# Kernel optimization log

Measured on AMD Instinct MI355X. Metric: run time of the kernel, lower is better.

Reference implementation:

```python
import jax, jax.numpy as jnp
import numpy as np

EMBED_DIM = 512
NUM_HEADS = 8
WINDOW = 5
OVERLAP = 1
STRIDE = WINDOW - OVERLAP  # 4


def setup_inputs() -> dict:
    key = jax.random.key(0)
    ks = jax.random.split(key, 5)
    B, S, D = 8, 4096, EMBED_DIM
    s = 1.0 / np.sqrt(D).astype(np.float32)
    return {
        "x": jax.random.normal(ks[0], (B, S, D), jnp.float32),
        "Wq": jax.random.normal(ks[1], (D, D), jnp.float32) * s,
        "bq": jnp.zeros((D,), jnp.float32),
        "Wk": jax.random.normal(ks[2], (D, D), jnp.float32) * s,
        "bk": jnp.zeros((D,), jnp.float32),
        "Wv": jax.random.normal(ks[3], (D, D), jnp.float32) * s,
        "bv": jnp.zeros((D,), jnp.float32),
        "Wo": jax.random.normal(ks[4], (D, D), jnp.float32) * s,
        "bo": jnp.zeros((D,), jnp.float32),
    }


def reference(x, Wq, bq, Wk, bk, Wv, bv, Wo, bo):
    B, S, D = x.shape
    H = NUM_HEADS
    hd = D // H
    pad = (WINDOW - S % WINDOW) % WINDOW
    xp = jnp.pad(x, ((0, 0), (0, pad), (0, 0)))
    P = S + pad
    nw = (P - WINDOW) // STRIDE + 1

    # gather all sliding windows at once: [B, nw, W, D]
    idx = (jnp.arange(nw) * STRIDE)[:, None] + jnp.arange(WINDOW)  # [nw, W]
    win = xp[:, idx]

    def proj(t, W, b):
        return (t @ W + b).reshape(B, nw, WINDOW, H, hd)

    q = proj(win, Wq, bq)
    k = proj(win, Wk, bk)
    v = proj(win, Wv, bv)

    scale = jnp.float32(1.0 / np.sqrt(hd))
    scores = jnp.einsum('bnqhd,bnkhd->bnhqk', q, k) * scale  # [B,nw,H,W,W]
    attn = jax.nn.softmax(scores, axis=-1)
    o = jnp.einsum('bnhqk,bnkhd->bnqhd', attn, v).reshape(B, nw, WINDOW, D)
    o = o @ Wo + bo  # window outputs [B,nw,W,D]

    # overlap-add + count-average (exactly as the torch loop does)
    flat_idx = idx.reshape(-1)
    out = jnp.zeros((B, P, D), jnp.float32).at[:, flat_idx].add(
        o.reshape(B, nw * WINDOW, D))
    counts = jnp.zeros((P,), jnp.float32).at[flat_idx].add(1.0)
    out = out / (counts[None, :, None] + 1e-6)
    out = out[:, :S]

    # torch: sum(all_weights) / num_windows  -> mean over window axis
    attn_weights = attn.mean(axis=1)  # [B, H, W, W]
    return out, attn_weights
```

## Files before the change

### kernel.cpp

```cpp
#include <hip/hip_runtime.h>
#include <hip/hip_bf16.h>


#define SEQ   4096
#define NB    8
#define DIM   512
#define NWIN  1024
#define MTOT  (NB*SEQ)

typedef __bf16 bf16x8 __attribute__((ext_vector_type(8)));
typedef float  f32x4  __attribute__((ext_vector_type(4)));

__device__ __forceinline__ float b2f(unsigned short u) {
  union { unsigned int i; float f; } z; z.i = ((unsigned int)u) << 16; return z.f;
}
__device__ __forceinline__ unsigned short f2b(float f) {
  __bf16 h = (__bf16)f; return __builtin_bit_cast(unsigned short, h);
}
__device__ __forceinline__ void gload_lds16(const void* g, void* l) {
  __builtin_amdgcn_global_load_lds(
      (__attribute__((address_space(1))) void*)g,
      (__attribute__((address_space(3))) void*)l, 16, 0, 0);
}

#define FENCE() asm volatile("" ::: "memory")
#define BAR()   __builtin_amdgcn_s_barrier()
#define VMW8()  asm volatile("s_waitcnt vmcnt(8)" ::: "memory")
#define VMW0()  asm volatile("s_waitcnt vmcnt(0)" ::: "memory")
#define LGK0()  asm volatile("s_waitcnt lgkmcnt(0)" ::: "memory")

__global__ __launch_bounds__(256) void cvt_x(const float* __restrict__ x,
                                             unsigned short* __restrict__ o, int n8) {
  int stride = gridDim.x * blockDim.x;
  for (int i = blockIdx.x * blockDim.x + threadIdx.x; i < n8; i += stride) {
    const float4 a = *(const float4*)(x + (size_t)i * 8);
    const float4 c = *(const float4*)(x + (size_t)i * 8 + 4);
    unsigned short u[8] = {f2b(a.x), f2b(a.y), f2b(a.z), f2b(a.w),
                           f2b(c.x), f2b(c.y), f2b(c.z), f2b(c.w)};
    *(int4*)(o + (size_t)i * 8) = *(const int4*)u;
  }
}

__global__ __launch_bounds__(256) void cvt_w(const float* __restrict__ W0, const float* __restrict__ W1,
                                             const float* __restrict__ W2, const float* __restrict__ W3,
                                             unsigned short* __restrict__ Wt) {
  int i = blockIdx.x * 256 + threadIdx.x;
  int w = i >> 18;
  int r = i & 262143;
  int nn = r >> 9, kk = r & 511;
  const float* W = (w == 0) ? W0 : (w == 1) ? W1 : (w == 2) ? W2 : W3;
  Wt[i] = f2b(W[kk * 512 + nn]);
}

__device__ __forceinline__ void stage_part(int h, const unsigned short* pa, const unsigned short* pb,
    int r0s, int c0s, int r1s, int c1s, char* ldsb, int wid) {
  int kt = h >> 2, slot = (h + 2) & 3;
  int buf = kt & 1, ab = slot >> 1, half = slot & 1;
  const unsigned short* src = ab ? pb : pa;
  int rb = half << 7;
  int kc = kt << 6;
  char* d = ldsb + buf * 65536 + ab * 32768 + half * 16384 + wid * 1024;
  gload_lds16(src + (size_t)(rb + r0s) * 512 + kc + c0s, d);
  gload_lds16(src + (size_t)(rb + r1s) * 512 + kc + c1s, d + 8192);
}

#define LDSB(off) (*(const bf16x8*)(ldsb + (off)))

#define RA4(BUF, HALF) { \
  _Pragma("unroll") for (int mf2 = 0; mf2 < 4; ++mf2) { \
    _Pragma("unroll") for (int ks = 0; ks < 2; ++ks) \
      a[mf2][ks] = LDSB(aS[BUF][ks] + (HALF) * 8192 + mf2 * 2048); } }

#define RB2(BUF, QN) { \
  _Pragma("unroll") for (int nf2 = 0; nf2 < 2; ++nf2) { \
    _Pragma("unroll") for (int ks = 0; ks < 2; ++ks) \
      b[(QN)*2+nf2][ks] = LDSB(bS[BUF][ks] + (QN) * 4096 + nf2 * 2048); } }

#define MMQ(QM, QN) { \
  _Pragma("unroll") for (int ks = 0; ks < 2; ++ks) \
  _Pragma("unroll") for (int mf2 = 0; mf2 < 4; ++mf2) \
  _Pragma("unroll") for (int nf2 = 0; nf2 < 2; ++nf2) \
    acc[(QM)*4+mf2][(QN)*2+nf2] = __builtin_amdgcn_mfma_f32_16x16x32_bf16( \
      a[mf2][ks], b[(QN)*2+nf2][ks], acc[(QM)*4+mf2][(QN)*2+nf2], 0, 0, 0); }

template<int MODE>
__global__ __launch_bounds__(512, 2) void gemm2p(
    const unsigned short* __restrict__ A, const unsigned short* __restrict__ Bw,
    const float* __restrict__ b0, const float* __restrict__ b1, const float* __restrict__ b2,
    unsigned short* __restrict__ o0, unsigned short* __restrict__ o1, unsigned short* __restrict__ o2,
    float* __restrict__ fout) {
  __shared__ unsigned short lds_[65536];
  char* ldsb = (char*)lds_;

  const int nwg = gridDim.x;
  const int cpx = nwg >> 3;
  const int g = blockIdx.x;
  const int sw = (g & 7) * cpx + (g >> 3);
  constexpr int NTN = (MODE == 0) ? 6 : 2;
  const int ntile = sw % NTN, mtile = sw / NTN;
  const int m0 = mtile * 256, n0g = ntile * 256;

  const int tid = threadIdx.x;
  const int lane = tid & 63;
  const int wid = tid >> 6;
  const int wr = wid >> 2, wc = wid & 3;
  const int cl16 = lane & 15, hi = lane >> 4;
  const int hi16 = hi * 16;
  const int sxor = (cl16 & 14) << 3;

  int o0_ = tid * 16;
  int o1_ = 8192 + tid * 16;
  int l0 = o0_ ^ (((o0_ >> 8) & 7) << 4);
  int l1 = o1_ ^ (((o1_ >> 8) & 7) << 4);
  const int r0s = l0 >> 7, c0s = (l0 & 127) >> 1;
  const int r1s = l1 >> 7, c1s = (l1 & 127) >> 1;

  const unsigned short* pa = A + (size_t)m0 * 512;
  const unsigned short* pb = Bw + (size_t)n0g * 512;

  int aS[2][2], bS[2][2];
#pragma unroll
  for (int bu = 0; bu < 2; ++bu)
#pragma unroll
    for (int ks = 0; ks < 2; ++ks) {
      aS[bu][ks] = bu * 65536 + ((wr * 16384 + cl16 * 128 + ks * 64 + hi16) ^ sxor);
      bS[bu][ks] = bu * 65536 + 32768 + (((wc >> 1) * 16384 + (wc & 1) * 8192 + cl16 * 128 + ks * 64 + hi16) ^ sxor);
    }

  f32x4 acc[8][4] = {};
  bf16x8 a[4][2], b[4][2];

#define STG4(KT) { stage_part((KT)*4, pa, pb, r0s, c0s, r1s, c1s, ldsb, wid); \
                   stage_part((KT)*4+1, pa, pb, r0s, c0s, r1s, c1s, ldsb, wid); \
                   stage_part((KT)*4+2, pa, pb, r0s, c0s, r1s, c1s, ldsb, wid); \
                   stage_part((KT)*4+3, pa, pb, r0s, c0s, r1s, c1s, ldsb, wid); }

  STG4(0);

#pragma unroll
  for (int kt = 0; kt < 8; ++kt) {
    const int bu = kt & 1;
    if (kt < 7) { STG4(kt + 1); VMW8(); } else { VMW0(); }
    FENCE(); BAR(); FENCE();
    RB2(bu, 0); RB2(bu, 1);
    RA4(bu, 0);
    MMQ(0, 0); MMQ(0, 1);
    RA4(bu, 1);
    MMQ(1, 1); MMQ(1, 0);
    FENCE(); BAR(); FENCE();
  }

  if constexpr (MODE == 0) {
    const int sel = n0g >> 9;
    const float* bias = (sel == 0) ? b0 : (sel == 1) ? b1 : b2;
    unsigned short* C = (sel == 0) ? o0 : (sel == 1) ? o1 : o2;
    const int lcb = (n0g & 511) + wc * 64;
    unsigned short* wlds = lds_ + wid * 8192;
#pragma unroll
    for (int mf = 0; mf < 8; ++mf)
#pragma unroll
      for (int nf = 0; nf < 4; ++nf) {
        float bv_ = bias[lcb + nf * 16 + cl16];
#pragma unroll
        for (int r = 0; r < 4; ++r) {
          int w = (mf * 16 + hi * 4 + r) * 64 + nf * 16 + cl16;
          wlds[w ^ (((w >> 7) & 7) << 3)] = f2b(acc[mf][nf][r] + bv_);
        }
      }
    LGK0();
#pragma unroll
    for (int itr = 0; itr < 16; ++itr) {
      int f = itr * 512 + lane * 8;
      int row = f >> 6, col = f & 63;
      int4 v = *(const int4*)&wlds[f ^ (((f >> 7) & 7) << 3)];
      *(int4*)(C + (size_t)(m0 + wr * 128 + row) * 512 + lcb + col) = v;
    }
  } else {
#pragma unroll
    for (int nf = 0; nf < 4; ++nf) {
      int ncol = n0g + wc * 64 + nf * 16 + cl16;
      float bv_ = b0[ncol];
#pragma unroll
      for (int mf = 0; mf < 8; ++mf) {
        int rbase = m0 + wr * 128 + mf * 16 + hi * 4;
#pragma unroll
        for (int r = 0; r < 4; ++r) {
          int row = rbase + r;
          int s = row & (SEQ - 1);
          float cnt = ((s & 3) == 0 && s > 0) ? 2.0f : 1.0f;
          fout[(size_t)row * 512 + ncol] = (acc[mf][nf][r] + cnt * bv_) / (cnt + 1e-6f);
        }
      }
    }
  }
}

__global__ __launch_bounds__(256) void attn_win(
    const unsigned short* __restrict__ Qb, const unsigned short* __restrict__ Kb,
    const unsigned short* __restrict__ Vb,
    const float* __restrict__ bq, const float* __restrict__ bk, const float* __restrict__ bv,
    unsigned short* __restrict__ yb, unsigned short* __restrict__ yext,
    float* __restrict__ abuf) {
  const int gw = blockIdx.x * 4 + (threadIdx.x >> 6);
  const int b = gw >> 10, n = gw & (NWIN - 1);
  const int lane = threadIdx.x & 63;
  const int h = lane >> 3, e = lane & 7;
  const int dbase = h * 64 + e * 8;

  float kf[5][8], vf[5][8];
#pragma unroll
  for (int j = 0; j < 5; ++j) {
    int p = 4 * n + j;
    if (p < SEQ) {
      int4 kv = *(const int4*)(Kb + ((size_t)b * SEQ + p) * DIM + dbase);
      int4 vv = *(const int4*)(Vb + ((size_t)b * SEQ + p) * DIM + dbase);
      const unsigned short* kp = (const unsigned short*)&kv;
      const unsigned short* vp = (const unsigned short*)&vv;
#pragma unroll
      for (int d = 0; d < 8; ++d) { kf[j][d] = b2f(kp[d]); vf[j][d] = b2f(vp[d]); }
    } else {
#pragma unroll
      for (int d = 0; d < 8; ++d) { kf[j][d] = bk[dbase + d]; vf[j][d] = bv[dbase + d]; }
    }
  }
  float pm[5][5];
#pragma unroll
  for (int i = 0; i < 5; ++i) {
    int p = 4 * n + i;
    float qf[8];
    if (p < SEQ) {
      int4 qv = *(const int4*)(Qb + ((size_t)b * SEQ + p) * DIM + dbase);
      const unsigned short* qp = (const unsigned short*)&qv;
#pragma unroll
      for (int d = 0; d < 8; ++d) qf[d] = b2f(qp[d]);
    } else {
#pragma unroll
      for (int d = 0; d < 8; ++d) qf[d] = bq[dbase + d];
    }
    float sr[5];
#pragma unroll
    for (int j = 0; j < 5; ++j) {
      float t = 0.f;
#pragma unroll
      for (int d = 0; d < 8; ++d) t += qf[d] * kf[j][d];
      t += __shfl_xor(t, 1);
      t += __shfl_xor(t, 2);
      t += __shfl_xor(t, 4);
      sr[j] = t * 0.125f;
    }
    float mx = sr[0];
#pragma unroll
    for (int j = 1; j < 5; ++j) mx = fmaxf(mx, sr[j]);
    float ex[5], sum = 0.f;
#pragma unroll
    for (int j = 0; j < 5; ++j) { ex[j] = expf(sr[j] - mx); sum += ex[j]; }
    float inv = 1.0f / sum;
#pragma unroll
    for (int j = 0; j < 5; ++j) pm[i][j] = ex[j] * inv;
    float o[8];
#pragma unroll
    for (int d = 0; d < 8; ++d) o[d] = 0.f;
#pragma unroll
    for (int j = 0; j < 5; ++j)
#pragma unroll
      for (int d = 0; d < 8; ++d) o[d] += pm[i][j] * vf[j][d];
    unsigned short u[8];
#pragma unroll
    for (int d = 0; d < 8; ++d) u[d] = f2b(o[d]);
    if (i < 4) {
      *(int4*)(yb + ((size_t)b * SEQ + p) * DIM + dbase) = *(const int4*)u;
    } else {
      *(int4*)(yext + ((size_t)b * NWIN + n) * DIM + dbase) = *(const int4*)u;
    }
  }
  float* ap = abuf + ((size_t)(b * NWIN + n) * 8 + h) * 25;
  if (e == 0) {
#pragma unroll
    for (int i2 = 0; i2 < 5; ++i2)
#pragma unroll
      for (int j2 = 0; j2 < 5; ++j2) ap[i2 * 5 + j2] = pm[i2][j2];
  }
}

__global__ __launch_bounds__(256) void merge_y(unsigned short* __restrict__ y,
                                               const unsigned short* __restrict__ ye) {
  int idx = blockIdx.x * 256 + threadIdx.x;
  if (idx >= 8 * 1023 * 64) return;
  int d8 = idx & 63;
  int t = idx >> 6;
  int n = t % 1023 + 1;
  int b = t / 1023;
  size_t yo = ((size_t)b * SEQ + 4 * (size_t)n) * DIM + d8 * 8;
  size_t eo = ((size_t)b * NWIN + (n - 1)) * DIM + d8 * 8;
  int4 av = *(const int4*)(y + yo);
  int4 cv = *(const int4*)(ye + eo);
  const unsigned short* ap = (const unsigned short*)&av;
  const unsigned short* cp = (const unsigned short*)&cv;
  unsigned short u[8];
#pragma unroll
  for (int j = 0; j < 8; ++j) u[j] = f2b(b2f(ap[j]) + b2f(cp[j]));
  *(int4*)(y + yo) = *(const int4*)u;
}

__global__ __launch_bounds__(256) void attn_reduce(const float* __restrict__ abuf,
                                                   float* __restrict__ out) {
  __shared__ float sm[256][25];
  int bh = blockIdx.x;
  int b = bh >> 3, h = bh & 7;
  int t = threadIdx.x;
  float loc[25];
#pragma unroll
  for (int j = 0; j < 25; ++j) loc[j] = 0.f;
  for (int n = t; n < NWIN; n += 256) {
    const float* p = abuf + ((size_t)(b * NWIN + n) * 8 + h) * 25;
#pragma unroll
    for (int j = 0; j < 25; ++j) loc[j] += p[j];
  }
#pragma unroll
  for (int j = 0; j < 25; ++j) sm[t][j] = loc[j];
  __syncthreads();
  for (int off = 128; off > 0; off >>= 1) {
    if (t < off)
#pragma unroll
      for (int j = 0; j < 25; ++j) sm[t][j] += sm[t + off][j];
    __syncthreads();
  }
  if (t < 25) out[bh * 25 + t] = sm[0][t] * (1.0f / 1024.0f);
}

extern "C" void kernel_launch(void* const* d_in, const int* in_sizes, int n_in,
                              void* d_out, int out_size, void* d_ws, size_t ws_size,
                              hipStream_t stream) {
  const float* x  = (const float*)d_in[0];
  const float* Wq = (const float*)d_in[1];
  const float* bq = (const float*)d_in[2];
  const float* Wk = (const float*)d_in[3];
  const float* bk = (const float*)d_in[4];
  const float* Wv = (const float*)d_in[5];
  const float* bv = (const float*)d_in[6];
  const float* Wo = (const float*)d_in[7];
  const float* bo = (const float*)d_in[8];
  float* out = (float*)d_out;

  char* ws = (char*)d_ws;
  unsigned short* xb   = (unsigned short*)(ws);
  unsigned short* yb   = xb;
  unsigned short* Qb   = (unsigned short*)(ws + 33554432);
  unsigned short* Kb   = (unsigned short*)(ws + 67108864);
  unsigned short* Vb   = (unsigned short*)(ws + 100663296);
  unsigned short* yext = (unsigned short*)(ws + 134217728);
  float*          abuf = (float*)(ws + 142606336);
  unsigned short* Wt   = (unsigned short*)(ws + 149159936);
  (void)ws_size; (void)in_sizes; (void)n_in; (void)out_size;

  cvt_x<<<2048, 256, 0, stream>>>(x, xb, MTOT * DIM / 8);
  cvt_w<<<4096, 256, 0, stream>>>(Wq, Wk, Wv, Wo, Wt);
  gemm2p<0><<<768, 512, 0, stream>>>(xb, Wt, bq, bk, bv, Qb, Kb, Vb, nullptr);
  attn_win<<<2048, 256, 0, stream>>>(Qb, Kb, Vb, bq, bk, bv, yb, yext, abuf);
  merge_y<<<2046, 256, 0, stream>>>(yb, yext);
  gemm2p<1><<<256, 512, 0, stream>>>(yb, Wt + 3 * (DIM * DIM), bo, nullptr, nullptr,
                                     nullptr, nullptr, nullptr, out);
  attn_reduce<<<64, 256, 0, stream>>>(abuf, out + (size_t)MTOT * DIM);
}
```

Baseline: 166.7 us.

## Split GEMM tile across 16 waves with smaller per-wave sub-tiles

The projection GEMMs now launch 1024 threads per 256x256 tile instead of 512. Each of 16 waves computes a 64x64 sub-tile with a 4x4 accumulator array instead of 128x64. Each thread issues one LDS-direct global load per stage part instead of two, and the wait count drops accordingly. This aims to raise wave-level parallelism and latency hiding and cut per-thread register pressure, at the cost of more redundant LDS fragment reads per MFMA and larger-block barrier sync. The launch bounds of 1024,4 may not be achievable with 128KB of LDS per block.

```diff
diff --git a/kernel.cpp b/kernel.cpp
--- a/kernel.cpp
+++ b/kernel.cpp
@@ -25,9 +25,9 @@
 
 #define FENCE() asm volatile("" ::: "memory")
 #define BAR()   __builtin_amdgcn_s_barrier()
-#define VMW8()  asm volatile("s_waitcnt vmcnt(8)" ::: "memory")
+#define LGK0()  asm volatile("s_waitcnt lgkmcnt(0)" ::: "memory")
+#define VMW4()  asm volatile("s_waitcnt vmcnt(4)" ::: "memory")
 #define VMW0()  asm volatile("s_waitcnt vmcnt(0)" ::: "memory")
-#define LGK0()  asm volatile("s_waitcnt lgkmcnt(0)" ::: "memory")
 
 __global__ __launch_bounds__(256) void cvt_x(const float* __restrict__ x,
                                              unsigned short* __restrict__ o, int n8) {
@@ -52,8 +52,8 @@
   Wt[i] = f2b(W[kk * 512 + nn]);
 }
 
-__device__ __forceinline__ void stage_part(int h, const unsigned short* pa, const unsigned short* pb,
-    int r0s, int c0s, int r1s, int c1s, char* ldsb, int wid) {
+__device__ __forceinline__ void stage_part16(int h, const unsigned short* pa, const unsigned short* pb,
+    int r0s, int c0s, char* ldsb, int wid) {
   int kt = h >> 2, slot = (h + 2) & 3;
   int buf = kt & 1, ab = slot >> 1, half = slot & 1;
   const unsigned short* src = ab ? pb : pa;
@@ -61,30 +61,26 @@
   int kc = kt << 6;
   char* d = ldsb + buf * 65536 + ab * 32768 + half * 16384 + wid * 1024;
   gload_lds16(src + (size_t)(rb + r0s) * 512 + kc + c0s, d);
-  gload_lds16(src + (size_t)(rb + r1s) * 512 + kc + c1s, d + 8192);
 }
 
 #define LDSB(off) (*(const bf16x8*)(ldsb + (off)))
 
-#define RA4(BUF, HALF) { \
-  _Pragma("unroll") for (int mf2 = 0; mf2 < 4; ++mf2) { \
-    _Pragma("unroll") for (int ks = 0; ks < 2; ++ks) \
-      a[mf2][ks] = LDSB(aS[BUF][ks] + (HALF) * 8192 + mf2 * 2048); } }
-
-#define RB2(BUF, QN) { \
-  _Pragma("unroll") for (int nf2 = 0; nf2 < 2; ++nf2) { \
-    _Pragma("unroll") for (int ks = 0; ks < 2; ++ks) \
-      b[(QN)*2+nf2][ks] = LDSB(bS[BUF][ks] + (QN) * 4096 + nf2 * 2048); } }
-
-#define MMQ(QM, QN) { \
-  _Pragma("unroll") for (int ks = 0; ks < 2; ++ks) \
-  _Pragma("unroll") for (int mf2 = 0; mf2 < 4; ++mf2) \
-  _Pragma("unroll") for (int nf2 = 0; nf2 < 2; ++nf2) \
-    acc[(QM)*4+mf2][(QN)*2+nf2] = __builtin_amdgcn_mfma_f32_16x16x32_bf16( \
-      a[mf2][ks], b[(QN)*2+nf2][ks], acc[(QM)*4+mf2][(QN)*2+nf2], 0, 0, 0); }
+#define RAX(BUF, KS) { \
+  _Pragma("unroll") for (int mf = 0; mf < 4; ++mf) \
+    a[mf] = LDSB(aS[BUF][KS] + mf * 2048); }
+
+#define RBX(BUF, KS) { \
+  _Pragma("unroll") for (int nf = 0; nf < 4; ++nf) \
+    b[nf] = LDSB(bS[BUF][KS] + nf * 2048); }
+
+#define MM16() { \
+  _Pragma("unroll") for (int mf = 0; mf < 4; ++mf) \
+  _Pragma("unroll") for (int nf = 0; nf < 4; ++nf) \
+    acc[mf][nf] = __builtin_amdgcn_mfma_f32_16x16x32_bf16( \
+      a[mf], b[nf], acc[mf][nf], 0, 0, 0); }
 
 template<int MODE>
-__global__ __launch_bounds__(512, 2) void gemm2p(
+__global__ __launch_bounds__(1024, 4) void gemm16(
     const unsigned short* __restrict__ A, const unsigned short* __restrict__ Bw,
     const float* __restrict__ b0, const float* __restrict__ b1, const float* __restrict__ b2,
     unsigned short* __restrict__ o0, unsigned short* __restrict__ o1, unsigned short* __restrict__ o2,
@@ -109,11 +105,8 @@
   const int sxor = (cl16 & 14) << 3;
 
   int o0_ = tid * 16;
-  int o1_ = 8192 + tid * 16;
   int l0 = o0_ ^ (((o0_ >> 8) & 7) << 4);
-  int l1 = o1_ ^ (((o1_ >> 8) & 7) << 4);
   const int r0s = l0 >> 7, c0s = (l0 & 127) >> 1;
-  const int r1s = l1 >> 7, c1s = (l1 & 127) >> 1;
 
   const unsigned short* pa = A + (size_t)m0 * 512;
   const unsigned short* pb = Bw + (size_t)n0g * 512;
@@ -123,30 +116,29 @@
   for (int bu = 0; bu < 2; ++bu)
 #pragma unroll
     for (int ks = 0; ks < 2; ++ks) {
-      aS[bu][ks] = bu * 65536 + ((wr * 16384 + cl16 * 128 + ks * 64 + hi16) ^ sxor);
-      bS[bu][ks] = bu * 65536 + 32768 + (((wc >> 1) * 16384 + (wc & 1) * 8192 + cl16 * 128 + ks * 64 + hi16) ^ sxor);
-    }
-
-  f32x4 acc[8][4] = {};
-  bf16x8 a[4][2], b[4][2];
-
-#define STG4(KT) { stage_part((KT)*4, pa, pb, r0s, c0s, r1s, c1s, ldsb, wid); \
-                   stage_part((KT)*4+1, pa, pb, r0s, c0s, r1s, c1s, ldsb, wid); \
-                   stage_part((KT)*4+2, pa, pb, r0s, c0s, r1s, c1s, ldsb, wid); \
-                   stage_part((KT)*4+3, pa, pb, r0s, c0s, r1s, c1s, ldsb, wid); }
+      aS[bu][ks] = bu * 65536 + ((wr * 8192 + cl16 * 128 + ks * 64 + hi16) ^ sxor);
+      bS[bu][ks] = bu * 65536 + 32768 + ((wc * 8192 + cl16 * 128 + ks * 64 + hi16) ^ sxor);
+    }
+
+  f32x4 acc[4][4] = {};
+  bf16x8 a[4], b[4];
+
+#define STG4(KT) { stage_part16((KT)*4,   pa, pb, r0s, c0s, ldsb, wid); \
+                   stage_part16((KT)*4+1, pa, pb, r0s, c0s, ldsb, wid); \
+                   stage_part16((KT)*4+2, pa, pb, r0s, c0s, ldsb, wid); \
+                   stage_part16((KT)*4+3, pa, pb, r0s, c0s, ldsb, wid); }
 
   STG4(0);
 
 #pragma unroll
   for (int kt = 0; kt < 8; ++kt) {
     const int bu = kt & 1;
-    if (kt < 7) { STG4(kt + 1); VMW8(); } else { VMW0(); }
+    if (kt < 7) { STG4(kt + 1); VMW4(); } else { VMW0(); }
     FENCE(); BAR(); FENCE();
-    RB2(bu, 0); RB2(bu, 1);
-    RA4(bu, 0);
-    MMQ(0, 0); MMQ(0, 1);
-    RA4(bu, 1);
-    MMQ(1, 1); MMQ(1, 0);
+    RAX(bu, 0); RBX(bu, 0);
+    MM16();
+    RAX(bu, 1); RBX(bu, 1);
+    MM16();
     FENCE(); BAR(); FENCE();
   }
 
@@ -155,9 +147,9 @@
     const float* bias = (sel == 0) ? b0 : (sel == 1) ? b1 : b2;
     unsigned short* C = (sel == 0) ? o0 : (sel == 1) ? o1 : o2;
     const int lcb = (n0g & 511) + wc * 64;
-    unsigned short* wlds = lds_ + wid * 8192;
-#pragma unroll
-    for (int mf = 0; mf < 8; ++mf)
+    unsigned short* wlds = lds_ + wid * 4096;
+#pragma unroll
+    for (int mf = 0; mf < 4; ++mf)
 #pragma unroll
       for (int nf = 0; nf < 4; ++nf) {
         float bv_ = bias[lcb + nf * 16 + cl16];
@@ -169,11 +161,11 @@
       }
     LGK0();
 #pragma unroll
-    for (int itr = 0; itr < 16; ++itr) {
+    for (int itr = 0; itr < 8; ++itr) {
       int f = itr * 512 + lane * 8;
       int row = f >> 6, col = f & 63;
       int4 v = *(const int4*)&wlds[f ^ (((f >> 7) & 7) << 3)];
-      *(int4*)(C + (size_t)(m0 + wr * 128 + row) * 512 + lcb + col) = v;
+      *(int4*)(C + (size_t)(m0 + wr * 64 + row) * 512 + lcb + col) = v;
     }
   } else {
 #pragma unroll
@@ -181,8 +173,8 @@
       int ncol = n0g + wc * 64 + nf * 16 + cl16;
       float bv_ = b0[ncol];
 #pragma unroll
-      for (int mf = 0; mf < 8; ++mf) {
-        int rbase = m0 + wr * 128 + mf * 16 + hi * 4;
+      for (int mf = 0; mf < 4; ++mf) {
+        int rbase = m0 + wr * 64 + mf * 16 + hi * 4;
 #pragma unroll
         for (int r = 0; r < 4; ++r) {
           int row = rbase + r;
@@ -355,10 +347,10 @@
 
   cvt_x<<<2048, 256, 0, stream>>>(x, xb, MTOT * DIM / 8);
   cvt_w<<<4096, 256, 0, stream>>>(Wq, Wk, Wv, Wo, Wt);
-  gemm2p<0><<<768, 512, 0, stream>>>(xb, Wt, bq, bk, bv, Qb, Kb, Vb, nullptr);
+  gemm16<0><<<768, 1024, 0, stream>>>(xb, Wt, bq, bk, bv, Qb, Kb, Vb, nullptr);
   attn_win<<<2048, 256, 0, stream>>>(Qb, Kb, Vb, bq, bk, bv, yb, yext, abuf);
   merge_y<<<2046, 256, 0, stream>>>(yb, yext);
-  gemm2p<1><<<256, 512, 0, stream>>>(yb, Wt + 3 * (DIM * DIM), bo, nullptr, nullptr,
-                                     nullptr, nullptr, nullptr, out);
+  gemm16<1><<<256, 1024, 0, stream>>>(yb, Wt + 3 * (DIM * DIM), bo, nullptr, nullptr,
+                                      nullptr, nullptr, nullptr, out);
   attn_reduce<<<64, 256, 0, stream>>>(abuf, out + (size_t)MTOT * DIM);
 }
```

After: 180.5 us. 8.3% more time.
